# Optimization experiments

Measured on AMD Instinct MI355X. Metric: run time of the kernel, lower is better.

Reference implementation:

```python
import jax, jax.numpy as jnp
import numpy as np

IN_F = 256
OUT_F = 64
LRELU_SLOPE = 0.2


def setup_inputs() -> dict:
    key = jax.random.key(0)
    k1, k2, k3 = jax.random.split(key, 3)
    B, N = 4, 4096
    h = jax.random.normal(k1, (B, N, IN_F), dtype=jnp.float32)
    # xavier_uniform with gain=1.414
    def xavier(k, shape, gain=1.414):
        fan_in, fan_out = shape[0], shape[1]
        bound = gain * np.sqrt(6.0 / (fan_in + fan_out))
        return jax.random.uniform(k, shape, jnp.float32, -bound, bound)
    W = xavier(k2, (IN_F, OUT_F))
    a = xavier(k3, (2 * OUT_F, 1))
    return {"h": h, "W": W, "a": a}


def reference(h, W, a):
    # Wh: (B, N, F_out)
    Wh = jnp.matmul(h, W)
    # Algebraic split of a = [a1; a2]: score(i,j) = Wh_i @ a1 + Wh_j @ a2
    a1 = a[:OUT_F, 0]   # (F,)
    a2 = a[OUT_F:, 0]   # (F,)
    e1 = Wh @ a1        # (B, N)
    e2 = Wh @ a2        # (B, N)
    e = e1[:, :, None] + e2[:, None, :]   # (B, N, N)
    return jnp.where(e > 0, e, LRELU_SLOPE * e)
```

## Files before the change

### kernel.cpp

```cpp
#include <hip/hip_runtime.h>
#include <hip/hip_bf16.h>


#define B_DIM 4
#define N_DIM 4096
#define IN_F 256
#define OUT_F 64
#define SLOPE 0.2f

typedef float f32x4 __attribute__((ext_vector_type(4)));

__global__ __launch_bounds__(256) void gat_dots(
        const float* __restrict__ h, const float* __restrict__ W,
        const float* __restrict__ a,
        float* __restrict__ e1, float* __restrict__ e2) {
    __shared__ float v1s[IN_F];
    __shared__ float v2s[IN_F];
    const int t    = threadIdx.x;
    const int lane = t & 63;
    const int wid  = t >> 6;

    {
        const int rgrp = lane >> 4;
        const int ch   = lane & 15;
        const f32x4 a1c = reinterpret_cast<const f32x4*>(a)[ch];
        const f32x4 a2c = reinterpret_cast<const f32x4*>(a + OUT_F)[ch];
        #pragma unroll
        for (int it = 0; it < 16; ++it) {
            const int row = wid * 64 + it * 4 + rgrp;
            const f32x4 wv = *reinterpret_cast<const f32x4*>(W + row * OUT_F + ch * 4);
            float s1 = wv.x * a1c.x + wv.y * a1c.y + wv.z * a1c.z + wv.w * a1c.w;
            float s2 = wv.x * a2c.x + wv.y * a2c.y + wv.z * a2c.z + wv.w * a2c.w;
            #pragma unroll
            for (int m = 8; m >= 1; m >>= 1) {
                s1 += __shfl_xor(s1, m);
                s2 += __shfl_xor(s2, m);
            }
            if (ch == 0) {
                v1s[row] = s1;
                v2s[row] = s2;
            }
        }
    }
    __syncthreads();

    const f32x4 v1 = reinterpret_cast<const f32x4*>(v1s)[lane];
    const f32x4 v2 = reinterpret_cast<const f32x4*>(v2s)[lane];
    const int base = blockIdx.x * 16 + wid * 4;

    #pragma unroll
    for (int r = 0; r < 4; ++r) {
        const int row = base + r;
        const f32x4 hv = reinterpret_cast<const f32x4*>(h + (size_t)row * IN_F)[lane];
        float d1 = hv.x * v1.x + hv.y * v1.y + hv.z * v1.z + hv.w * v1.w;
        float d2 = hv.x * v2.x + hv.y * v2.y + hv.z * v2.z + hv.w * v2.w;
        #pragma unroll
        for (int m = 32; m >= 1; m >>= 1) {
            d1 += __shfl_xor(d1, m);
            d2 += __shfl_xor(d2, m);
        }
        if (lane == 0) {
            e1[row] = d1;
            e2[row] = d2;
        }
    }
}

__global__ __launch_bounds__(256) void gat_epilogue(
        const float* __restrict__ e1, const float* __restrict__ e2,
        float* __restrict__ out) {
    const int rowBase = blockIdx.x * 8;
    const int b       = rowBase >> 12;
    const int tid     = threadIdx.x;

    const f32x4* e2v = reinterpret_cast<const f32x4*>(e2 + b * N_DIM);
    const f32x4 c0 = e2v[tid];
    const f32x4 c1 = e2v[tid + 256];
    const f32x4 c2 = e2v[tid + 512];
    const f32x4 c3 = e2v[tid + 768];

    float s[8];
    #pragma unroll
    for (int r = 0; r < 8; ++r) s[r] = e1[rowBase + r];

    #pragma unroll
    for (int r = 0; r < 8; ++r) {
        f32x4* outv = reinterpret_cast<f32x4*>(out + (size_t)(rowBase + r) * N_DIM);
        f32x4 o0, o1, o2, o3;
        #define LRELU(dst, src) { \
            float ex = s[r] + (src).x; (dst).x = fmaxf(ex, SLOPE * ex); \
            float ey = s[r] + (src).y; (dst).y = fmaxf(ey, SLOPE * ey); \
            float ez = s[r] + (src).z; (dst).z = fmaxf(ez, SLOPE * ez); \
            float ew = s[r] + (src).w; (dst).w = fmaxf(ew, SLOPE * ew); }
        LRELU(o0, c0) LRELU(o1, c1) LRELU(o2, c2) LRELU(o3, c3)
        #undef LRELU
        outv[tid]       = o0;
        outv[tid + 256] = o1;
        outv[tid + 512] = o2;
        outv[tid + 768] = o3;
    }
}

extern "C" void kernel_launch(void* const* d_in, const int* in_sizes, int n_in,
                              void* d_out, int out_size, void* d_ws, size_t ws_size,
                              hipStream_t stream) {
    const float* h = (const float*)d_in[0];
    const float* W = (const float*)d_in[1];
    const float* a = (const float*)d_in[2];

    float* ws = (float*)d_ws;
    float* e1 = ws;
    float* e2 = ws + 16384;

    gat_dots<<<1024, 256, 0, stream>>>(h, W, a, e1, e2);
    gat_epilogue<<<2048, 256, 0, stream>>>(e1, e2, (float*)d_out);
}
```

Before: 60.93 us.

## Fuse dot and epilogue kernels into one cooperative kernel with grid sync

Merges the projection-dot kernel and the LeakyReLU broadcast epilogue into a single cooperative launch of 1024 blocks. Each block keeps its 16 e1 values in shared memory and publishes e2 to global memory, then waits on a grid-wide barrier before writing its 16 output rows. This removes one kernel launch and the global round trip for e1. In exchange it adds a grid-sync cost, halves the number of epilogue blocks, and relies on all 1024 blocks being co-resident, which the launch bound of 4 blocks per CU is meant to guarantee.

```diff
diff --git a/kernel.cpp b/kernel.cpp
--- a/kernel.cpp
+++ b/kernel.cpp
@@ -1,5 +1,8 @@
 #include <hip/hip_runtime.h>
 #include <hip/hip_bf16.h>
+#include <hip/hip_cooperative_groups.h>
+
+namespace cg = cooperative_groups;
 
 
 #define B_DIM 4
@@ -10,15 +13,18 @@
 
 typedef float f32x4 __attribute__((ext_vector_type(4)));
 
-__global__ __launch_bounds__(256) void gat_dots(
+__global__ __launch_bounds__(256, 4) void gat_fused(
         const float* __restrict__ h, const float* __restrict__ W,
         const float* __restrict__ a,
-        float* __restrict__ e1, float* __restrict__ e2) {
+        float* __restrict__ e2g, float* __restrict__ out) {
     __shared__ float v1s[IN_F];
     __shared__ float v2s[IN_F];
+    __shared__ float e1s[16];
+
     const int t    = threadIdx.x;
     const int lane = t & 63;
     const int wid  = t >> 6;
+    const int bid  = blockIdx.x;
 
     {
         const int rgrp = lane >> 4;
@@ -44,47 +50,44 @@
     }
     __syncthreads();
 
-    const f32x4 v1 = reinterpret_cast<const f32x4*>(v1s)[lane];
-    const f32x4 v2 = reinterpret_cast<const f32x4*>(v2s)[lane];
-    const int base = blockIdx.x * 16 + wid * 4;
+    {
+        const f32x4 v1 = reinterpret_cast<const f32x4*>(v1s)[lane];
+        const f32x4 v2 = reinterpret_cast<const f32x4*>(v2s)[lane];
+        #pragma unroll
+        for (int r = 0; r < 4; ++r) {
+            const int lr  = wid * 4 + r;
+            const int row = bid * 16 + lr;
+            const f32x4 hv = reinterpret_cast<const f32x4*>(h + (size_t)row * IN_F)[lane];
+            float d1 = hv.x * v1.x + hv.y * v1.y + hv.z * v1.z + hv.w * v1.w;
+            float d2 = hv.x * v2.x + hv.y * v2.y + hv.z * v2.z + hv.w * v2.w;
+            #pragma unroll
+            for (int m = 32; m >= 1; m >>= 1) {
+                d1 += __shfl_xor(d1, m);
+                d2 += __shfl_xor(d2, m);
+            }
+            if (lane == 0) {
+                e1s[lr]   = d1;
+                e2g[row]  = d2;
+            }
+        }
+    }
+    __threadfence();
+    cg::this_grid().sync();
+
+    const int rowBase = bid * 16;
+    const int b       = rowBase >> 12;
+    const f32x4* e2v  = reinterpret_cast<const f32x4*>(e2g + b * N_DIM);
+    const f32x4 c0 = e2v[t];
+    const f32x4 c1 = e2v[t + 256];
+    const f32x4 c2 = e2v[t + 512];
+    const f32x4 c3 = e2v[t + 768];
+
+    float s[16];
+    #pragma unroll
+    for (int r = 0; r < 16; ++r) s[r] = e1s[r];
 
     #pragma unroll
-    for (int r = 0; r < 4; ++r) {
-        const int row = base + r;
-        const f32x4 hv = reinterpret_cast<const f32x4*>(h + (size_t)row * IN_F)[lane];
-        float d1 = hv.x * v1.x + hv.y * v1.y + hv.z * v1.z + hv.w * v1.w;
-        float d2 = hv.x * v2.x + hv.y * v2.y + hv.z * v2.z + hv.w * v2.w;
-        #pragma unroll
-        for (int m = 32; m >= 1; m >>= 1) {
-            d1 += __shfl_xor(d1, m);
-            d2 += __shfl_xor(d2, m);
-        }
-        if (lane == 0) {
-            e1[row] = d1;
-            e2[row] = d2;
-        }
-    }
-}
-
-__global__ __launch_bounds__(256) void gat_epilogue(
-        const float* __restrict__ e1, const float* __restrict__ e2,
-        float* __restrict__ out) {
-    const int rowBase = blockIdx.x * 8;
-    const int b       = rowBase >> 12;
-    const int tid     = threadIdx.x;
-
-    const f32x4* e2v = reinterpret_cast<const f32x4*>(e2 + b * N_DIM);
-    const f32x4 c0 = e2v[tid];
-    const f32x4 c1 = e2v[tid + 256];
-    const f32x4 c2 = e2v[tid + 512];
-    const f32x4 c3 = e2v[tid + 768];
-
-    float s[8];
-    #pragma unroll
-    for (int r = 0; r < 8; ++r) s[r] = e1[rowBase + r];
-
-    #pragma unroll
-    for (int r = 0; r < 8; ++r) {
+    for (int r = 0; r < 16; ++r) {
         f32x4* outv = reinterpret_cast<f32x4*>(out + (size_t)(rowBase + r) * N_DIM);
         f32x4 o0, o1, o2, o3;
         #define LRELU(dst, src) { \
@@ -94,10 +97,10 @@
             float ew = s[r] + (src).w; (dst).w = fmaxf(ew, SLOPE * ew); }
         LRELU(o0, c0) LRELU(o1, c1) LRELU(o2, c2) LRELU(o3, c3)
         #undef LRELU
-        outv[tid]       = o0;
-        outv[tid + 256] = o1;
-        outv[tid + 512] = o2;
-        outv[tid + 768] = o3;
+        outv[t]       = o0;
+        outv[t + 256] = o1;
+        outv[t + 512] = o2;
+        outv[t + 768] = o3;
     }
 }
 
@@ -107,11 +110,9 @@
     const float* h = (const float*)d_in[0];
     const float* W = (const float*)d_in[1];
     const float* a = (const float*)d_in[2];
+    float* e2g = (float*)d_ws;
+    float* out = (float*)d_out;
 
-    float* ws = (float*)d_ws;
-    float* e1 = ws;
-    float* e2 = ws + 16384;
-
-    gat_dots<<<1024, 256, 0, stream>>>(h, W, a, e1, e2);
-    gat_epilogue<<<2048, 256, 0, stream>>>(e1, e2, (float*)d_out);
+    void* args[] = { (void*)&h, (void*)&W, (void*)&a, (void*)&e2g, (void*)&out };
+    hipLaunchCooperativeKernel((void*)gat_fused, dim3(1024), dim3(256), args, 0, stream);
 }
```

After: 213.0 us. +249.6%, slower.

## Restructure epilogue into persistent column-strided grid looping over rows and batches

Applied to the files above, without the earlier changes.

The broadcast-add plus LeakyReLU epilogue now runs on 256 blocks instead of 2048. Each thread owns one float4 column slot, keeps its e2 value in a register for each batch, and walks 64 rows with a stride of 64, prefetching the next e1 scalar. The aim is to cut block scheduling overhead and redundant e2 reloads in this write-bandwidth-bound output stage. The cost is lower occupancy, only about four waves per CU, to hide store latency. The last prefetch reads slightly past each batch's e1 slice into the neighbouring workspace, which is harmless but untidy.

```diff
diff --git a/kernel.cpp b/kernel.cpp
--- a/kernel.cpp
+++ b/kernel.cpp
@@ -36,10 +36,7 @@
                 s1 += __shfl_xor(s1, m);
                 s2 += __shfl_xor(s2, m);
             }
-            if (ch == 0) {
-                v1s[row] = s1;
-                v2s[row] = s2;
-            }
+            if (ch == 0) { v1s[row] = s1; v2s[row] = s2; }
         }
     }
     __syncthreads();
@@ -59,45 +56,35 @@
             d1 += __shfl_xor(d1, m);
             d2 += __shfl_xor(d2, m);
         }
-        if (lane == 0) {
-            e1[row] = d1;
-            e2[row] = d2;
-        }
+        if (lane == 0) { e1[row] = d1; e2[row] = d2; }
     }
 }
 
 __global__ __launch_bounds__(256) void gat_epilogue(
         const float* __restrict__ e1, const float* __restrict__ e2,
         float* __restrict__ out) {
-    const int rowBase = blockIdx.x * 8;
-    const int b       = rowBase >> 12;
-    const int tid     = threadIdx.x;
+    const int g    = blockIdx.x * 256 + threadIdx.x;
+    const int col4 = g & 1023;
+    const int row0 = g >> 10;
 
-    const f32x4* e2v = reinterpret_cast<const f32x4*>(e2 + b * N_DIM);
-    const f32x4 c0 = e2v[tid];
-    const f32x4 c1 = e2v[tid + 256];
-    const f32x4 c2 = e2v[tid + 512];
-    const f32x4 c3 = e2v[tid + 768];
+    for (int b = 0; b < B_DIM; ++b) {
+        const f32x4 c = reinterpret_cast<const f32x4*>(e2 + b * N_DIM)[col4];
+        const float* e1b = e1 + b * N_DIM;
+        f32x4* outb = reinterpret_cast<f32x4*>(out + (size_t)b * N_DIM * N_DIM);
 
-    float s[8];
-    #pragma unroll
-    for (int r = 0; r < 8; ++r) s[r] = e1[rowBase + r];
-
-    #pragma unroll
-    for (int r = 0; r < 8; ++r) {
-        f32x4* outv = reinterpret_cast<f32x4*>(out + (size_t)(rowBase + r) * N_DIM);
-        f32x4 o0, o1, o2, o3;
-        #define LRELU(dst, src) { \
-            float ex = s[r] + (src).x; (dst).x = fmaxf(ex, SLOPE * ex); \
-            float ey = s[r] + (src).y; (dst).y = fmaxf(ey, SLOPE * ey); \
-            float ez = s[r] + (src).z; (dst).z = fmaxf(ez, SLOPE * ez); \
-            float ew = s[r] + (src).w; (dst).w = fmaxf(ew, SLOPE * ew); }
-        LRELU(o0, c0) LRELU(o1, c1) LRELU(o2, c2) LRELU(o3, c3)
-        #undef LRELU
-        outv[tid]       = o0;
-        outv[tid + 256] = o1;
-        outv[tid + 512] = o2;
-        outv[tid + 768] = o3;
+        float s = e1b[row0];
+        #pragma unroll 4
+        for (int it = 0; it < 64; ++it) {
+            const int row = row0 + it * 64;
+            const float snext = e1b[row + 64];
+            f32x4 o;
+            float ex = s + c.x; o.x = fmaxf(ex, SLOPE * ex);
+            float ey = s + c.y; o.y = fmaxf(ey, SLOPE * ey);
+            float ez = s + c.z; o.z = fmaxf(ez, SLOPE * ez);
+            float ew = s + c.w; o.w = fmaxf(ew, SLOPE * ew);
+            outb[(size_t)row * (N_DIM / 4) + col4] = o;
+            s = snext;
+        }
     }
 }
 
@@ -113,5 +100,5 @@
     float* e2 = ws + 16384;
 
     gat_dots<<<1024, 256, 0, stream>>>(h, W, a, e1, e2);
-    gat_epilogue<<<2048, 256, 0, stream>>>(e1, e2, (float*)d_out);
+    gat_epilogue<<<256, 256, 0, stream>>>(e1, e2, (float*)d_out);
 }
```

After: 60.32 us. Within noise of the previous version (-1.0%).
